# Performance work log

Hardware: AMD Instinct MI355X
Metric: run time of the kernel (lower is better)

Reference implementation:

```python
import jax, jax.numpy as jnp
import numpy as np
from jax import lax

B, C, N, NB = 64, 512, 1024, 4
BC = C // NB
KS = [3, 5, 7, 9]
LEVEL = 2  # min(2, pywt.dwt_max_level(1024, 8)) = 2
FL = 8  # db4 filter length
DN = ('NCH', 'OIH', 'NCH')
# pywt db4 decomposition filters
DEC_LO = jnp.array([-0.010597401784997278, 0.032883011666982945, 0.030841381835986965,
                    -0.18703481171888114, -0.02798376941698385, 0.6308807679295904,
                    0.7148465705525415, 0.23037781330885523], jnp.float32)
DEC_HI = jnp.array([-0.23037781330885523, 0.7148465705525415, -0.6308807679295904,
                    -0.02798376941698385, 0.18703481171888114, 0.030841381835986965,
                    -0.032883011666982945, -0.010597401784997278], jnp.float32)


def conv1d(x, w, b, pad):
    y = lax.conv_general_dilated(x, w, (1,), [(pad, pad)], dimension_numbers=DN)
    return y + b[None, :, None]


def bn_relu(x, g, beta, eps=1e-5):
    # BatchNorm1d in train mode: batch statistics over (B, L) per channel
    mu = x.mean(axis=(0, 2), keepdims=True)
    var = ((x - mu) ** 2).mean(axis=(0, 2), keepdims=True)
    xn = (x - mu) * lax.rsqrt(var + eps)
    return jax.nn.relu(xn * g[None, :, None] + beta[None, :, None])


def dwt1d(x):
    # single-level pywt-compatible DWT, symmetric mode. x: [B, C, n]
    b, c, n = x.shape
    out = (n + FL - 1) // 2
    p = 2 * (out - 1) - n + FL
    xp = jnp.pad(x, ((0, 0), (0, 0), (p // 2, p - p // 2)), mode='symmetric')
    k = jnp.stack([DEC_LO[::-1], DEC_HI[::-1]])[:, None, :]  # [2,1,FL]
    y = lax.conv_general_dilated(xp.reshape(b * c, 1, -1), k, (2,), 'VALID',
                                 dimension_numbers=DN)
    y = y.reshape(b, c, 2, out)
    return y[:, :, 0], y[:, :, 1]  # (cA, cD)


def idwt1d(lo, hi):
    # single-level inverse DWT; output length = 2*nc - FL + 2
    b, c, nc = lo.shape
    x = jnp.stack([lo, hi], axis=2).reshape(b * c, 2, nc)
    # rec filters = dec filters reversed, so flipped-for-conv == dec filters
    k = jnp.stack([DEC_LO, DEC_HI])[None, :, :]  # [1,2,FL]
    y = lax.conv_general_dilated(x, k, (1,), [(FL - 1, FL - 1)],
                                 lhs_dilation=(2,), dimension_numbers=DN)
    y = y[:, 0, FL - 2: FL - 2 + 2 * nc - FL + 2]
    return y.reshape(b, c, -1)


def decouple(x):
    # TemporalPatternDecoupling: db4 wavedec(level=2) -> reconstruct low-pass-only
    # (long term) and detail-only (short term). Torch detaches before pywt.
    x = lax.stop_gradient(x)
    n = x.shape[-1]
    a, details = x, []
    for _ in range(LEVEL):
        a, d = dwt1d(a)
        details.append(d)
    la, sa = a, jnp.zeros_like(a)
    for d in reversed(details):
        dl = d.shape[-1]
        la = idwt1d(la[..., :dl], jnp.zeros_like(d))
        sa = idwt1d(sa[..., :dl], d)
    return sa[..., :n], la[..., :n]


def setup_inputs() -> dict:
    key = jax.random.key(0)
    ks = jax.random.split(key, 32)
    s = 0.05
    inp = {
        'x': jax.random.normal(ks[0], (B, C, N), jnp.float32),
        'w_init': jax.random.normal(ks[1], (C, C, 1), jnp.float32) * s,
        'b_init': jnp.zeros((C,), jnp.float32),
        'w_pf': jax.random.normal(ks[2], (BC, 2 * BC, 1), jnp.float32) * s,
        'b_pf': jnp.zeros((BC,), jnp.float32),
        'w_fus': jax.random.normal(ks[3], (C, C, 1), jnp.float32) * s,
        'b_fus': jnp.zeros((C,), jnp.float32),
    }
    for i in range(NB):
        inp[f'w_b{i + 1}'] = jax.random.normal(ks[4 + i], (BC, BC, KS[i]), jnp.float32) * s
        inp[f'b_b{i + 1}'] = jnp.zeros((BC,), jnp.float32)
        inp[f'g_b{i + 1}'] = jnp.ones((BC,), jnp.float32)
        inp[f'be_b{i + 1}'] = jnp.zeros((BC,), jnp.float32)
    return inp


def reference(x, w_init, b_init, w_b1, b_b1, g_b1, be_b1, w_b2, b_b2, g_b2, be_b2,
              w_b3, b_b3, g_b3, be_b3, w_b4, b_b4, g_b4, be_b4, w_pf, b_pf,
              w_fus, b_fus):
    identity = x
    h = conv1d(x, w_init, b_init, 0)
    branch_in = jnp.split(h, NB, axis=1)
    wb = [w_b1, w_b2, w_b3, w_b4]
    bb = [b_b1, b_b2, b_b3, b_b4]
    gb = [g_b1, g_b2, g_b3, g_b4]
    beb = [be_b1, be_b2, be_b3, be_b4]
    shorts, longs = [], []
    for i in range(NB):
        y = bn_relu(conv1d(branch_in[i], wb[i], bb[i], KS[i] // 2), gb[i], beb[i])
        s, l = decouple(y)
        shorts.append(s)
        longs.append(l)
    for b in range(1, NB):
        shorts[b] = shorts[b] + shorts[b - 1]
    for b in range(NB - 2, -1, -1):
        longs[b] = longs[b] + longs[b + 1]
    enhanced = [conv1d(jnp.concatenate([shorts[b], longs[b]], axis=1), w_pf, b_pf, 0)
                for b in range(NB)]
    out = conv1d(jnp.concatenate(enhanced, axis=1), w_fus, b_fus, 0)
    return out + identity
```

## Files before the change

### kernel.cpp

```cpp
#include <hip/hip_runtime.h>

typedef float  f32x4 __attribute__((ext_vector_type(4)));
typedef short  s16x8 __attribute__((ext_vector_type(8)));
typedef short  s16x4 __attribute__((ext_vector_type(4)));
typedef unsigned short u16;

struct PtrQuad { const float* p[4]; };

__constant__ float c_lo[8] = {-0.010597401784997278f, 0.032883011666982945f,
                              0.030841381835986965f, -0.18703481171888114f,
                              -0.02798376941698385f, 0.6308807679295904f,
                              0.7148465705525415f,  0.23037781330885523f};
__constant__ float c_hi[8] = {-0.23037781330885523f, 0.7148465705525415f,
                              -0.6308807679295904f, -0.02798376941698385f,
                              0.18703481171888114f, 0.030841381835986965f,
                              -0.032883011666982945f, -0.010597401784997278f};

__device__ __forceinline__ u16 f2bf(float f) {
    unsigned u = __float_as_uint(f);
    u += 0x7fffu + ((u >> 16) & 1u);
    return (u16)(u >> 16);
}
__device__ __forceinline__ float bf2f(u16 h) {
    return __uint_as_float(((unsigned)h) << 16);
}
__device__ __forceinline__ int lds_chunk(int row, int g) {
    return row * 4 + (g ^ ((row >> 1) & 3));
}
__device__ __forceinline__ void gload16(void* lds, const void* g) {
    __builtin_amdgcn_global_load_lds(
        (__attribute__((address_space(1))) const void*)g,
        (__attribute__((address_space(3))) void*)lds,
        16, 0, 0);
}
__device__ __forceinline__ void pipe_wait2(int t, int nt) {
    if (t + 1 < nt) asm volatile("s_waitcnt vmcnt(4)" ::: "memory");
    else            asm volatile("s_waitcnt vmcnt(0)" ::: "memory");
    __builtin_amdgcn_s_barrier();
    __builtin_amdgcn_sched_barrier(0);
}
__device__ __forceinline__ void pipe_endbar() {
    __builtin_amdgcn_sched_barrier(0);
    __builtin_amdgcn_s_barrier();
}

__global__ __launch_bounds__(256) void gemm_nt_k(
    const u16* __restrict__ A, long aB, int lda,
    const u16* __restrict__ B, long bB, int ldb,
    int K,
    u16* __restrict__ D, long dB, int dj,
    const float* __restrict__ bias)
{
    __shared__ s16x8 As[2 * 512];
    __shared__ s16x8 Bs[2 * 512];
    int flat = blockIdx.x + 8 * (blockIdx.y + 4 * blockIdx.z);
    int swz = (flat & 7) * 256 + (flat >> 3);
    const int j0 = (swz & 7) * 128;
    const int i0 = ((swz >> 3) & 3) * 128;
    const long bb = swz >> 5;
    const u16* Ab = A + bb * aB;
    const u16* Bb = B + bb * bB;
    const int tid = threadIdx.x;
    const int srow = tid >> 2, sg = tid & 3;
    const int ssg = sg ^ ((srow >> 1) & 3);
    const int l = tid & 63, w = tid >> 6;
    const int wi = (w >> 1) * 64, wj = (w & 1) * 64;
    const int lr = l & 15, lg = l >> 4;
    const long aoff0 = (long)(i0 + srow) * lda + ssg * 8;
    const long aoff1 = (long)(i0 + srow + 64) * lda + ssg * 8;
    const long boff0 = (long)(j0 + srow) * ldb + ssg * 8;
    const long boff1 = (long)(j0 + srow + 64) * ldb + ssg * 8;
    const int nt = K >> 5;
    auto stage = [&](int buf, int t) {
        const int k0 = t << 5;
        char* a0 = (char*)As + buf * 8192 + w * 1024;
        char* b0 = (char*)Bs + buf * 8192 + w * 1024;
        gload16(a0, Ab + aoff0 + k0);
        gload16(a0 + 4096, Ab + aoff1 + k0);
        gload16(b0, Bb + boff0 + k0);
        gload16(b0 + 4096, Bb + boff1 + k0);
    };
    f32x4 acc[4][4] = {};
    stage(0, 0);
    for (int t = 0; t < nt; ++t) {
        const int cur = t & 1;
        if (t + 1 < nt) stage(cur ^ 1, t + 1);
        pipe_wait2(t, nt);
        s16x8 af[4], bf[4];
        #pragma unroll
        for (int f = 0; f < 4; ++f) {
            af[f] = As[cur * 512 + lds_chunk(wi + f * 16 + lr, lg)];
            bf[f] = Bs[cur * 512 + lds_chunk(wj + f * 16 + lr, lg)];
        }
        #pragma unroll
        for (int fi = 0; fi < 4; ++fi)
            #pragma unroll
            for (int fj = 0; fj < 4; ++fj)
                acc[fi][fj] = __builtin_amdgcn_mfma_f32_16x16x32_bf16(af[fi], bf[fj], acc[fi][fj], 0, 0, 0);
        pipe_endbar();
    }
    u16* Db = D + bb * dB;
    #pragma unroll
    for (int fi = 0; fi < 4; ++fi) {
        const int i = i0 + wi + fi * 16 + lg * 4;
        float b0 = 0, b1 = 0, b2v = 0, b3 = 0;
        if (bias) { b0 = bias[i]; b1 = bias[i + 1]; b2v = bias[i + 2]; b3 = bias[i + 3]; }
        #pragma unroll
        for (int fj = 0; fj < 4; ++fj) {
            const int j = j0 + wj + fj * 16 + lr;
            f32x4 d = acc[fi][fj];
            s16x4 o;
            o[0] = (short)f2bf(d[0] + b0); o[1] = (short)f2bf(d[1] + b1);
            o[2] = (short)f2bf(d[2] + b2v); o[3] = (short)f2bf(d[3] + b3);
            *(s16x4*)(Db + (long)j * dj + i) = o;
        }
    }
}

__global__ __launch_bounds__(256) void gemm_branch4_k(
    const u16* __restrict__ WpAll,
    const u16* __restrict__ H,
    u16* __restrict__ Y,
    const u16* __restrict__ zbuf,
    float* __restrict__ part)
{
    __shared__ s16x8 As[2 * 512];
    __shared__ s16x8 Bs[2 * 512];
    __shared__ float sred[2][128];
    __shared__ float qred[2][128];
    int flat = blockIdx.x + 8 * (blockIdx.y + 4 * blockIdx.z);
    int swz = (flat & 7) * 256 + (flat >> 3);
    const int jblk = swz & 7;
    const int br = (swz >> 3) & 3;
    const long bb = swz >> 5;
    const int j0 = jblk * 128;
    const int taps = 3 + 2 * br;
    const int pad = 1 + br;
    const u16* Wp = WpAll + (long)(br * br + 2 * br) * 16384;
    const u16* Hb = H + bb * 524288 + 128 * br;
    const int tid = threadIdx.x;
    const int srow = tid >> 2, sg = tid & 3;
    const int ssg = sg ^ ((srow >> 1) & 3);
    const int l = tid & 63, w = tid >> 6;
    const int wi = (w >> 1) * 64, wj = (w & 1) * 64;
    const int lr = l & 15, lg = l >> 4;
    const int lda = taps * 128;
    const int nt = taps * 4;
    auto stage = [&](int buf, int t) {
        const int k0 = t << 5;
        const int tap = k0 >> 7, kc = k0 & 127;
        const int shift = tap - pad;
        char* a0 = (char*)As + buf * 8192 + w * 1024;
        char* b0 = (char*)Bs + buf * 8192 + w * 1024;
        gload16(a0, Wp + (long)srow * lda + k0 + ssg * 8);
        gload16(a0 + 4096, Wp + (long)(srow + 64) * lda + k0 + ssg * 8);
        int n0r = j0 + srow + shift;
        int n1r = n0r + 64;
        const u16* s0 = (n0r >= 0 && n0r < 1024) ? (Hb + (long)n0r * 512 + kc + ssg * 8) : zbuf;
        const u16* s1 = (n1r >= 0 && n1r < 1024) ? (Hb + (long)n1r * 512 + kc + ssg * 8) : zbuf;
        gload16(b0, s0);
        gload16(b0 + 4096, s1);
    };
    f32x4 acc[4][4] = {};
    stage(0, 0);
    for (int t = 0; t < nt; ++t) {
        const int cur = t & 1;
        if (t + 1 < nt) stage(cur ^ 1, t + 1);
        pipe_wait2(t, nt);
        s16x8 af[4], bf[4];
        #pragma unroll
        for (int f = 0; f < 4; ++f) {
            af[f] = As[cur * 512 + lds_chunk(wi + f * 16 + lr, lg)];
            bf[f] = Bs[cur * 512 + lds_chunk(wj + f * 16 + lr, lg)];
        }
        #pragma unroll
        for (int fi = 0; fi < 4; ++fi)
            #pragma unroll
            for (int fj = 0; fj < 4; ++fj)
                acc[fi][fj] = __builtin_amdgcn_mfma_f32_16x16x32_bf16(af[fi], bf[fj], acc[fi][fj], 0, 0, 0);
        pipe_endbar();
    }
    u16* Db = Y + bb * 524288 + 128 * br;
    #pragma unroll
    for (int fi = 0; fi < 4; ++fi) {
        const int i = wi + fi * 16 + lg * 4;
        #pragma unroll
        for (int fj = 0; fj < 4; ++fj) {
            const int j = j0 + wj + fj * 16 + lr;
            f32x4 d = acc[fi][fj];
            s16x4 o;
            o[0] = (short)f2bf(d[0]); o[1] = (short)f2bf(d[1]);
            o[2] = (short)f2bf(d[2]); o[3] = (short)f2bf(d[3]);
            *(s16x4*)(Db + (long)j * 512 + i) = o;
        }
    }
    float sv[16], qv[16];
    #pragma unroll
    for (int fi = 0; fi < 4; ++fi)
        #pragma unroll
        for (int e = 0; e < 4; ++e) {
            float s = 0.f, q = 0.f;
            #pragma unroll
            for (int fj = 0; fj < 4; ++fj) { float d = acc[fi][fj][e]; s += d; q += d * d; }
            sv[fi * 4 + e] = s; qv[fi * 4 + e] = q;
        }
    #pragma unroll
    for (int m = 1; m < 16; m <<= 1) {
        #pragma unroll
        for (int r = 0; r < 16; ++r) {
            sv[r] += __shfl_xor(sv[r], m, 64);
            qv[r] += __shfl_xor(qv[r], m, 64);
        }
    }
    __syncthreads();
    if (lr == 0) {
        #pragma unroll
        for (int r = 0; r < 16; ++r) {
            int co = wi + (r >> 2) * 16 + lg * 4 + (r & 3);
            sred[w & 1][co] = sv[r];
            qred[w & 1][co] = qv[r];
        }
    }
    __syncthreads();
    if (tid < 128) {
        long blk = (long)br * 512 + bb * 8 + jblk;
        part[blk * 256 + tid]       = sred[0][tid] + sred[1][tid];
        part[blk * 256 + 128 + tid] = qred[0][tid] + qred[1][tid];
    }
}

__global__ __launch_bounds__(256) void gemm_psl_k(
    const u16* __restrict__ Ybn,
    const u16* __restrict__ Bmat,
    u16* __restrict__ PSL)
{
    __shared__ s16x8 As[2 * 512];
    __shared__ s16x8 Bs[2 * 512];
    int flat = blockIdx.x + 8 * (blockIdx.y + 8 * blockIdx.z);
    int swz = (flat & 7) * 512 + (flat >> 3);
    const int j0 = (swz & 7) * 128;
    const int i0 = ((swz >> 3) & 7) * 128;
    const long bb = swz >> 6;
    const int tid = threadIdx.x;
    const u16* Ab = Ybn + bb * 524288;
    const int srow = tid >> 2, sg = tid & 3;
    const int ssg = sg ^ ((srow >> 1) & 3);
    const int l = tid & 63, w = tid >> 6;
    const int wi = (w >> 1) * 64, wj = (w & 1) * 64;
    const int lr = l & 15, lg = l >> 4;
    const long aoff0 = (long)(i0 + srow) * 512 + ssg * 8;
    const long aoff1 = (long)(i0 + srow + 64) * 512 + ssg * 8;
    const long boff0 = (long)(j0 + srow) * 512 + ssg * 8;
    const long boff1 = (long)(j0 + srow + 64) * 512 + ssg * 8;
    const int nt = 16;
    auto stage = [&](int buf, int t) {
        const int k0 = t << 5;
        char* a0 = (char*)As + buf * 8192 + w * 1024;
        char* b0 = (char*)Bs + buf * 8192 + w * 1024;
        gload16(a0, Ab + aoff0 + k0);
        gload16(a0 + 4096, Ab + aoff1 + k0);
        gload16(b0, Bmat + boff0 + k0);
        gload16(b0 + 4096, Bmat + boff1 + k0);
    };
    f32x4 acc[4][4] = {};
    stage(0, 0);
    for (int t = 0; t < nt; ++t) {
        const int cur = t & 1;
        if (t + 1 < nt) stage(cur ^ 1, t + 1);
        pipe_wait2(t, nt);
        s16x8 af[4], bf[4];
        #pragma unroll
        for (int f = 0; f < 4; ++f) {
            af[f] = As[cur * 512 + lds_chunk(wi + f * 16 + lr, lg)];
            bf[f] = Bs[cur * 512 + lds_chunk(wj + f * 16 + lr, lg)];
        }
        #pragma unroll
        for (int fi = 0; fi < 4; ++fi)
            #pragma unroll
            for (int fj = 0; fj < 4; ++fj)
                acc[fi][fj] = __builtin_amdgcn_mfma_f32_16x16x32_bf16(af[fi], bf[fj], acc[fi][fj], 0, 0, 0);
        pipe_endbar();
    }
    u16* Db = PSL + bb * 1048576;
    #pragma unroll
    for (int fi = 0; fi < 4; ++fi) {
        const int i = i0 + wi + fi * 16 + lg * 4;
        #pragma unroll
        for (int fj = 0; fj < 4; ++fj) {
            const int j = j0 + wj + fj * 16 + lr;
            f32x4 d = acc[fi][fj];
            s16x4 o;
            o[0] = (short)f2bf(d[0]); o[1] = (short)f2bf(d[1]);
            o[2] = (short)f2bf(d[2]); o[3] = (short)f2bf(d[3]);
            *(s16x4*)(Db + (long)j * 1024 + i) = o;
        }
    }
}

__global__ __launch_bounds__(256) void gemm_time_k(
    const u16* __restrict__ MS,
    const u16* __restrict__ PSL,
    const float* __restrict__ b2, const float* __restrict__ X,
    float* __restrict__ OUT)
{
    __shared__ s16x8 As[2 * 512];
    __shared__ s16x8 Bs[2 * 512];
    int flat = blockIdx.x + 4 * (blockIdx.y + 8 * blockIdx.z);
    int swz = (flat & 7) * 256 + (flat >> 3);
    const int j0 = (swz & 3) * 128;
    const int i0 = ((swz >> 2) & 7) * 128;
    const long bb = swz >> 5;
    const int tid = threadIdx.x;
    const int srow = tid >> 2, sg = tid & 3;
    const int ssg = sg ^ ((srow >> 1) & 3);
    const int l = tid & 63, w = tid >> 6;
    const int wi = (w >> 1) * 64, wj = (w & 1) * 64;
    const int lr = l & 15, lg = l >> 4;
    const int klo = (i0 - 32) > 0 ? (i0 - 32) : 0;
    const int khi = (i0 + 160) < 1024 ? (i0 + 160) : 1024;
    const int nt = (khi - klo) >> 5;
    const u16* B = PSL + bb * 1048576;
    auto stage = [&](int buf, int t) {
        const int k0 = klo + (t << 5);
        char* a0 = (char*)As + buf * 8192 + w * 1024;
        char* b0 = (char*)Bs + buf * 8192 + w * 1024;
        gload16(a0, MS + (long)(i0 + srow) * 1024 + k0 + ssg * 8);
        gload16(a0 + 4096, MS + (long)(i0 + srow + 64) * 1024 + k0 + ssg * 8);
        gload16(b0, B + (long)(j0 + srow) * 1024 + k0 + ssg * 8);
        gload16(b0 + 4096, B + (long)(j0 + srow + 64) * 1024 + k0 + ssg * 8);
    };
    f32x4 acc[4][4] = {};
    stage(0, 0);
    for (int t = 0; t < nt; ++t) {
        const int cur = t & 1;
        if (t + 1 < nt) stage(cur ^ 1, t + 1);
        pipe_wait2(t, nt);
        s16x8 af[4], bf[4];
        #pragma unroll
        for (int f = 0; f < 4; ++f) {
            af[f] = As[cur * 512 + lds_chunk(wi + f * 16 + lr, lg)];
            bf[f] = Bs[cur * 512 + lds_chunk(wj + f * 16 + lr, lg)];
        }
        #pragma unroll
        for (int fi = 0; fi < 4; ++fi)
            #pragma unroll
            for (int fj = 0; fj < 4; ++fj)
                acc[fi][fj] = __builtin_amdgcn_mfma_f32_16x16x32_bf16(af[fi], bf[fj], acc[fi][fj], 0, 0, 0);
        pipe_endbar();
    }
    float* Ob = OUT + bb * 524288;
    const float* Xb = X + bb * 524288;
    const u16* PLb = PSL + bb * 1048576 + 524288;
    #pragma unroll
    for (int fi = 0; fi < 4; ++fi) {
        const int i = i0 + wi + fi * 16 + lg * 4;
        #pragma unroll
        for (int fj = 0; fj < 4; ++fj) {
            const int j = j0 + wj + fj * 16 + lr;
            const long a = (long)j * 1024 + i;
            f32x4 d = acc[fi][fj];
            const float bj = b2[j];
            f32x4 xv = *(const f32x4*)(Xb + a);
            s16x4 pl4 = *(const s16x4*)(PLb + a);
            f32x4 o;
            o[0] = d[0] + bj + xv[0] + bf2f((u16)pl4[0]);
            o[1] = d[1] + bj + xv[1] + bf2f((u16)pl4[1]);
            o[2] = d[2] + bj + xv[2] + bf2f((u16)pl4[2]);
            o[3] = d[3] + bj + xv[3] + bf2f((u16)pl4[3]);
            *(f32x4*)(Ob + a) = o;
        }
    }
}

__global__ __launch_bounds__(256) void build_M_k(u16* __restrict__ MS)
{
    __shared__ float a1[515], d1[515], a2[261], d2[261], sa1[515];
    const int r = blockIdx.x;
    const int t = threadIdx.x;
    for (int m = t; m < 515; m += 256) {
        float sa = 0.f, sd = 0.f;
        #pragma unroll
        for (int j = 0; j < 8; ++j) {
            int tt = 2 * m + 1 - j;
            tt = (tt < 0) ? (-tt - 1) : tt;
            tt = (tt >= 1024) ? (2047 - tt) : tt;
            if (tt == r) { sa += c_lo[j]; sd += c_hi[j]; }
        }
        a1[m] = sa; d1[m] = sd;
    }
    __syncthreads();
    for (int m = t; m < 261; m += 256) {
        float sa = 0.f, sd = 0.f;
        #pragma unroll
        for (int j = 0; j < 8; ++j) {
            int tt = 2 * m + 1 - j;
            tt = (tt < 0) ? (-tt - 1) : tt;
            tt = (tt >= 515) ? (1029 - tt) : tt;
            float v = a1[tt];
            sa += v * c_lo[j]; sd += v * c_hi[j];
        }
        a2[m] = sa; d2[m] = sd;
    }
    __syncthreads();
    for (int m = t; m < 515; m += 256) {
        float ss = 0.f;
        #pragma unroll
        for (int k = 0; k < 8; ++k) {
            int tt = m + k - 1;
            if (tt & 1) continue;
            int j = tt >> 1;
            if (j < 0 || j >= 261) continue;
            ss += c_hi[k] * d2[j];
        }
        sa1[m] = ss;
    }
    __syncthreads();
    for (int n = t; n < 1024; n += 256) {
        float ss = 0.f;
        #pragma unroll
        for (int k = 0; k < 8; ++k) {
            int tt = n + k - 1;
            if (tt & 1) continue;
            int j = tt >> 1;
            if (j < 0 || j >= 515) continue;
            ss += c_lo[k] * sa1[j] + c_hi[k] * d1[j];
        }
        MS[(long)n * 1024 + r] = f2bf(ss);
    }
}

__global__ __launch_bounds__(256) void pack_weights_k(
    const float* __restrict__ wi,
    const float* __restrict__ b1, const float* __restrict__ b2_,
    const float* __restrict__ b3, const float* __restrict__ b4,
    u16* __restrict__ Wi, u16* __restrict__ Wp)
{
    int i = blockIdx.x * 256 + threadIdx.x;
    if (i < 262144) Wi[i] = f2bf(wi[i]);
    if (i < 393216) {
        int base, taps;
        const float* s;
        if (i < 49152)       { base = 0;      taps = 3; s = b1; }
        else if (i < 131072) { base = 49152;  taps = 5; s = b2_; }
        else if (i < 245760) { base = 131072; taps = 7; s = b3; }
        else                 { base = 245760; taps = 9; s = b4; }
        int rem = i - base;
        int stride = taps * 128;
        int co = rem / stride;
        int r2 = rem - co * stride;
        int tap = r2 >> 7, ci = r2 & 127;
        Wp[i] = f2bf(s[(long)(co * 128 + ci) * taps + tap]);
    }
}

__global__ __launch_bounds__(256) void make_Ucum_k(
    const float* __restrict__ wf, const float* __restrict__ wp,
    u16* __restrict__ UDUL)
{
    int gid = blockIdx.x * 256 + threadIdx.x;
    int co = gid >> 7, cc = gid & 127;
    float us[4], ul[4];
    #pragma unroll
    for (int b = 0; b < 4; ++b) {
        float s = 0.f, t = 0.f;
        for (int q = 0; q < 128; ++q) {
            float f = wf[(long)co * 512 + b * 128 + q];
            s += f * wp[q * 256 + cc];
            t += f * wp[q * 256 + 128 + cc];
        }
        us[b] = s; ul[b] = t;
    }
    float suf[4], pre[4];
    float acc = 0.f;
    for (int b = 3; b >= 0; --b) { acc += us[b]; suf[b] = acc; }
    acc = 0.f;
    for (int b = 0; b < 4; ++b) { acc += ul[b]; pre[b] = acc; }
    #pragma unroll
    for (int b = 0; b < 4; ++b) {
        UDUL[(long)co * 512 + b * 128 + cc]         = f2bf(suf[b] - pre[b]);
        UDUL[(long)(512 + co) * 512 + b * 128 + cc] = f2bf(pre[b]);
    }
}

__global__ __launch_bounds__(256) void make_bias2_k(
    const float* __restrict__ wf, const float* __restrict__ bpf,
    const float* __restrict__ bfus, float* __restrict__ b2)
{
    int co = blockIdx.x * 256 + threadIdx.x;
    if (co >= 512) return;
    float s = bfus[co];
    for (int j = 0; j < 512; ++j) s += wf[(long)co * 512 + j] * bpf[j & 127];
    b2[co] = s;
}

__global__ __launch_bounds__(256) void zero_k(float* __restrict__ p, int n)
{
    int i = blockIdx.x * 256 + threadIdx.x;
    if (i < n) p[i] = 0.f;
}

__global__ __launch_bounds__(256) void trX_k(const float* __restrict__ x, u16* __restrict__ xcl)
{
    __shared__ float sh[32][33];
    const int n0 = blockIdx.x * 32, c0 = blockIdx.y * 32;
    const long bb = blockIdx.z;
    const int tx = threadIdx.x, ty = threadIdx.y;
    const float* xb = x + bb * 524288;
    u16* ob = xcl + bb * 524288;
    #pragma unroll
    for (int k = 0; k < 4; ++k)
        sh[ty + 8 * k][tx] = xb[(long)(c0 + ty + 8 * k) * 1024 + n0 + tx];
    __syncthreads();
    #pragma unroll
    for (int k = 0; k < 4; ++k)
        ob[(long)(n0 + ty + 8 * k) * 512 + c0 + tx] = f2bf(sh[tx][ty + 8 * k]);
}

__global__ __launch_bounds__(256) void bn_coef_k(
    const float* __restrict__ part, PtrQuad g, PtrQuad be, float* __restrict__ scsh)
{
    int c = blockIdx.x * 256 + threadIdx.x;
    if (c >= 512) return;
    int br = c >> 7, cc = c & 127;
    const float* pb = part + (long)br * 131072;
    float s = 0.f, q = 0.f;
    for (int pidx = 0; pidx < 512; ++pidx) {
        s += pb[pidx * 256 + cc];
        q += pb[pidx * 256 + 128 + cc];
    }
    float mu = s * (1.0f / 65536.0f);
    float var = q * (1.0f / 65536.0f) - mu * mu;
    float sc = g.p[br][cc] * rsqrtf(var + 1e-5f);
    scsh[c] = sc;
    scsh[512 + c] = be.p[br][cc] - mu * sc;
}

__global__ __launch_bounds__(256) void bn_apply_k(
    u16* __restrict__ Y, const float* __restrict__ scsh)
{
    __shared__ float sc_[512];
    __shared__ float sh_[512];
    const int t = threadIdx.x;
    #pragma unroll
    for (int q = 0; q < 2; ++q) {
        sc_[t + q * 256] = scsh[t + q * 256];
        sh_[t + q * 256] = scsh[512 + t + q * 256];
    }
    __syncthreads();
    long gid = (long)blockIdx.x * 256 + t;
    long r = gid >> 6; int cg = (int)(gid & 63);
    u16* p = Y + r * 512 + cg * 8;
    s16x8 v = *(const s16x8*)p;
    #pragma unroll
    for (int e = 0; e < 8; ++e) {
        int c = cg * 8 + e;
        float f = bf2f((u16)v[e]) * sc_[c] + sh_[c];
        v[e] = (short)f2bf(f > 0.f ? f : 0.f);
    }
    *(s16x8*)p = v;
}

extern "C" void kernel_launch(void* const* d_in, const int* in_sizes, int n_in,
                              void* d_out, int out_size, void* d_ws, size_t ws_size,
                              hipStream_t stream)
{
    const float* x      = (const float*)d_in[0];
    const float* w_init = (const float*)d_in[1];
    const float* b_init = (const float*)d_in[2];
    const float* w_pf   = (const float*)d_in[3];
    const float* b_pf   = (const float*)d_in[4];
    const float* w_fus  = (const float*)d_in[5];
    const float* b_fus  = (const float*)d_in[6];
    const float *w_b[4];
    PtrQuad g, be;
    for (int i = 0; i < 4; ++i) {
        w_b[i]  = (const float*)d_in[7 + 4 * i];
        g.p[i]  = (const float*)d_in[9 + 4 * i];
        be.p[i] = (const float*)d_in[10 + 4 * i];
    }
    float* outf = (float*)d_out;

    char* p = (char*)d_ws;
    u16* xcl   = (u16*)p;  p += 67108864;
    u16* h     = (u16*)p;  p += 67108864;
    u16* Y     = (u16*)p;  p += 67108864;
    u16* PSL   = (u16*)p;  p += 134217728;
    u16* Wi    = (u16*)p;  p += 524288;
    u16* Wp    = (u16*)p;  p += 786432;
    u16* UDUL  = (u16*)p;  p += 1048576;
    u16* MrowS = (u16*)p;  p += 2097152;
    float* b2  = (float*)p; p += 2048;
    float* zbuf= (float*)p; p += 256;
    float* scsh= (float*)p; p += 4096;
    float* part= (float*)p; p += 2097152;

    pack_weights_k<<<1536, 256, 0, stream>>>(w_init, w_b[0], w_b[1], w_b[2], w_b[3], Wi, Wp);
    make_Ucum_k<<<256, 256, 0, stream>>>(w_fus, w_pf, UDUL);
    make_bias2_k<<<2, 256, 0, stream>>>(w_fus, b_pf, b_fus, b2);
    build_M_k<<<1024, 256, 0, stream>>>(MrowS);
    zero_k<<<1, 256, 0, stream>>>(zbuf, 64);

    trX_k<<<dim3(32, 16, 64), dim3(32, 8), 0, stream>>>(x, xcl);

    gemm_nt_k<<<dim3(8, 4, 64), 256, 0, stream>>>(Wi, 0, 512, xcl, 524288, 512, 512,
                                                  h, 524288, 512, b_init);

    gemm_branch4_k<<<dim3(8, 4, 64), 256, 0, stream>>>(Wp, h, Y, (const u16*)zbuf, part);

    bn_coef_k<<<2, 256, 0, stream>>>(part, g, be, scsh);
    bn_apply_k<<<16384, 256, 0, stream>>>(Y, scsh);

    gemm_psl_k<<<dim3(8, 8, 64), 256, 0, stream>>>(Y, UDUL, PSL);

    gemm_time_k<<<dim3(4, 8, 64), 256, 0, stream>>>(MrowS, PSL, b2, x, outf);
}
```

Measured before the change: 503.7 us.

## Reuse H window across conv taps, parallelize BN stats, raise MFMA priority

Measured after the change: 476.5 us. -5.4%, faster.

```diff
diff --git a/kernel.cpp b/kernel.cpp
--- a/kernel.cpp
+++ b/kernel.cpp
@@ -92,11 +92,13 @@
             af[f] = As[cur * 512 + lds_chunk(wi + f * 16 + lr, lg)];
             bf[f] = Bs[cur * 512 + lds_chunk(wj + f * 16 + lr, lg)];
         }
+        __builtin_amdgcn_s_setprio(1);
         #pragma unroll
         for (int fi = 0; fi < 4; ++fi)
             #pragma unroll
             for (int fj = 0; fj < 4; ++fj)
                 acc[fi][fj] = __builtin_amdgcn_mfma_f32_16x16x32_bf16(af[fi], bf[fj], acc[fi][fj], 0, 0, 0);
+        __builtin_amdgcn_s_setprio(0);
         pipe_endbar();
     }
     u16* Db = D + bb * dB;
@@ -124,8 +126,8 @@
     const u16* __restrict__ zbuf,
     float* __restrict__ part)
 {
-    __shared__ s16x8 As[2 * 512];
-    __shared__ s16x8 Bs[2 * 512];
+    __shared__ char Alds[2 * 8192];
+    __shared__ char Blds[2 * 12288];
     __shared__ float sred[2][128];
     __shared__ float qred[2][128];
     int flat = blockIdx.x + 8 * (blockIdx.y + 4 * blockIdx.z);
@@ -136,49 +138,78 @@
     const int j0 = jblk * 128;
     const int taps = 3 + 2 * br;
     const int pad = 1 + br;
-    const u16* Wp = WpAll + (long)(br * br + 2 * br) * 16384;
+    const u16* Wpb = WpAll + (long)(br * br + 2 * br) * 16384;
     const u16* Hb = H + bb * 524288 + 128 * br;
     const int tid = threadIdx.x;
-    const int srow = tid >> 2, sg = tid & 3;
-    const int ssg = sg ^ ((srow >> 1) & 3);
     const int l = tid & 63, w = tid >> 6;
     const int wi = (w >> 1) * 64, wj = (w & 1) * 64;
     const int lr = l & 15, lg = l >> 4;
+    const int lrow = l >> 2, lq = l & 3;
+    const int ssg2 = lq ^ ((lrow >> 1) & 3);
     const int lda = taps * 128;
-    const int nt = taps * 4;
-    auto stage = [&](int buf, int t) {
-        const int k0 = t << 5;
-        const int tap = k0 >> 7, kc = k0 & 127;
-        const int shift = tap - pad;
-        char* a0 = (char*)As + buf * 8192 + w * 1024;
-        char* b0 = (char*)Bs + buf * 8192 + w * 1024;
-        gload16(a0, Wp + (long)srow * lda + k0 + ssg * 8);
-        gload16(a0 + 4096, Wp + (long)(srow + 64) * lda + k0 + ssg * 8);
-        int n0r = j0 + srow + shift;
-        int n1r = n0r + 64;
-        const u16* s0 = (n0r >= 0 && n0r < 1024) ? (Hb + (long)n0r * 512 + kc + ssg * 8) : zbuf;
-        const u16* s1 = (n1r >= 0 && n1r < 1024) ? (Hb + (long)n1r * 512 + kc + ssg * 8) : zbuf;
-        gload16(b0, s0);
-        gload16(b0 + 4096, s1);
+
+    auto stageA = [&](int buf, int c, int t) {
+        char* dst = Alds + buf * 8192 + w * 2048;
+        #pragma unroll
+        for (int q = 0; q < 2; ++q) {
+            int row = w * 32 + q * 16 + lrow;
+            gload16(dst + q * 1024,
+                    Wpb + (long)row * lda + t * 128 + c * 32 + ssg2 * 8);
+        }
     };
+    auto stageB = [&](int buf, int c) {
+        char* dst = Blds + buf * 12288 + w * 3072;
+        #pragma unroll
+        for (int q = 0; q < 3; ++q) {
+            int winrow = w * 48 + q * 16 + lrow;
+            int grow = j0 - 32 + winrow;
+            const u16* src = (grow >= 0 && grow < 1024)
+                           ? (Hb + (long)grow * 512 + c * 32 + ssg2 * 8) : zbuf;
+            gload16(dst + q * 1024, src);
+        }
+    };
+
     f32x4 acc[4][4] = {};
-    stage(0, 0);
-    for (int t = 0; t < nt; ++t) {
-        const int cur = t & 1;
-        if (t + 1 < nt) stage(cur ^ 1, t + 1);
-        pipe_wait2(t, nt);
-        s16x8 af[4], bf[4];
-        #pragma unroll
-        for (int f = 0; f < 4; ++f) {
-            af[f] = As[cur * 512 + lds_chunk(wi + f * 16 + lr, lg)];
-            bf[f] = Bs[cur * 512 + lds_chunk(wj + f * 16 + lr, lg)];
-        }
-        #pragma unroll
-        for (int fi = 0; fi < 4; ++fi)
+    int abuf = 0, bbuf = 0;
+    stageB(0, 0);
+    stageA(0, 0, 0);
+    for (int c = 0; c < 4; ++c) {
+        for (int t = 0; t < taps; ++t) {
+            if (t + 1 < taps) {
+                stageA(abuf ^ 1, c, t + 1);
+                asm volatile("s_waitcnt vmcnt(2)" ::: "memory");
+            } else if (c + 1 < 4) {
+                stageB(bbuf ^ 1, c + 1);
+                stageA(abuf ^ 1, c + 1, 0);
+                asm volatile("s_waitcnt vmcnt(5)" ::: "memory");
+            } else {
+                asm volatile("s_waitcnt vmcnt(0)" ::: "memory");
+            }
+            __builtin_amdgcn_s_barrier();
+            __builtin_amdgcn_sched_barrier(0);
+            const char* Al = Alds + abuf * 8192;
+            const char* Bl = Blds + bbuf * 12288;
+            const int shift2 = t - pad + 32;
+            s16x8 af[4], bf[4];
             #pragma unroll
-            for (int fj = 0; fj < 4; ++fj)
-                acc[fi][fj] = __builtin_amdgcn_mfma_f32_16x16x32_bf16(af[fi], bf[fj], acc[fi][fj], 0, 0, 0);
-        pipe_endbar();
+            for (int f = 0; f < 4; ++f) {
+                int arow = wi + f * 16 + lr;
+                af[f] = *(const s16x8*)(Al + arow * 64 + (lg ^ ((arow >> 1) & 3)) * 16);
+                int brow = wj + f * 16 + lr + shift2;
+                bf[f] = *(const s16x8*)(Bl + brow * 64 + (lg ^ ((brow >> 1) & 3)) * 16);
+            }
+            __builtin_amdgcn_s_setprio(1);
+            #pragma unroll
+            for (int fi = 0; fi < 4; ++fi)
+                #pragma unroll
+                for (int fj = 0; fj < 4; ++fj)
+                    acc[fi][fj] = __builtin_amdgcn_mfma_f32_16x16x32_bf16(af[fi], bf[fj], acc[fi][fj], 0, 0, 0);
+            __builtin_amdgcn_s_setprio(0);
+            __builtin_amdgcn_sched_barrier(0);
+            __builtin_amdgcn_s_barrier();
+            abuf ^= 1;
+            if (t == taps - 1) bbuf ^= 1;
+        }
     }
     u16* Db = Y + bb * 524288 + 128 * br;
     #pragma unroll
@@ -274,11 +305,13 @@
             af[f] = As[cur * 512 + lds_chunk(wi + f * 16 + lr, lg)];
             bf[f] = Bs[cur * 512 + lds_chunk(wj + f * 16 + lr, lg)];
         }
+        __builtin_amdgcn_s_setprio(1);
         #pragma unroll
         for (int fi = 0; fi < 4; ++fi)
             #pragma unroll
             for (int fj = 0; fj < 4; ++fj)
                 acc[fi][fj] = __builtin_amdgcn_mfma_f32_16x16x32_bf16(af[fi], bf[fj], acc[fi][fj], 0, 0, 0);
+        __builtin_amdgcn_s_setprio(0);
         pipe_endbar();
     }
     u16* Db = PSL + bb * 1048576;
@@ -341,11 +374,13 @@
             af[f] = As[cur * 512 + lds_chunk(wi + f * 16 + lr, lg)];
             bf[f] = Bs[cur * 512 + lds_chunk(wj + f * 16 + lr, lg)];
         }
+        __builtin_amdgcn_s_setprio(1);
         #pragma unroll
         for (int fi = 0; fi < 4; ++fi)
             #pragma unroll
             for (int fj = 0; fj < 4; ++fj)
                 acc[fi][fj] = __builtin_amdgcn_mfma_f32_16x16x32_bf16(af[fi], bf[fj], acc[fi][fj], 0, 0, 0);
+        __builtin_amdgcn_s_setprio(0);
         pipe_endbar();
     }
     float* Ob = OUT + bb * 524288;
@@ -519,20 +554,26 @@
 __global__ __launch_bounds__(256) void bn_coef_k(
     const float* __restrict__ part, PtrQuad g, PtrQuad be, float* __restrict__ scsh)
 {
-    int c = blockIdx.x * 256 + threadIdx.x;
-    if (c >= 512) return;
+    __shared__ float rs[256], rq[256];
+    int c = blockIdx.x;
     int br = c >> 7, cc = c & 127;
     const float* pb = part + (long)br * 131072;
-    float s = 0.f, q = 0.f;
-    for (int pidx = 0; pidx < 512; ++pidx) {
-        s += pb[pidx * 256 + cc];
-        q += pb[pidx * 256 + 128 + cc];
-    }
-    float mu = s * (1.0f / 65536.0f);
-    float var = q * (1.0f / 65536.0f) - mu * mu;
-    float sc = g.p[br][cc] * rsqrtf(var + 1e-5f);
-    scsh[c] = sc;
-    scsh[512 + c] = be.p[br][cc] - mu * sc;
+    int t = threadIdx.x;
+    float s = pb[(2 * t) * 256 + cc]       + pb[(2 * t + 1) * 256 + cc];
+    float q = pb[(2 * t) * 256 + 128 + cc] + pb[(2 * t + 1) * 256 + 128 + cc];
+    rs[t] = s; rq[t] = q;
+    __syncthreads();
+    for (int off = 128; off > 0; off >>= 1) {
+        if (t < off) { rs[t] += rs[t + off]; rq[t] += rq[t + off]; }
+        __syncthreads();
+    }
+    if (t == 0) {
+        float mu = rs[0] * (1.0f / 65536.0f);
+        float var = rq[0] * (1.0f / 65536.0f) - mu * mu;
+        float sc = g.p[br][cc] * rsqrtf(var + 1e-5f);
+        scsh[c] = sc;
+        scsh[512 + c] = be.p[br][cc] - mu * sc;
+    }
 }
 
 __global__ __launch_bounds__(256) void bn_apply_k(
@@ -607,7 +648,7 @@
 
     gemm_branch4_k<<<dim3(8, 4, 64), 256, 0, stream>>>(Wp, h, Y, (const u16*)zbuf, part);
 
-    bn_coef_k<<<2, 256, 0, stream>>>(part, g, be, scsh);
+    bn_coef_k<<<512, 256, 0, stream>>>(part, g, be, scsh);
     bn_apply_k<<<16384, 256, 0, stream>>>(Y, scsh);
 
     gemm_psl_k<<<dim3(8, 8, 64), 256, 0, stream>>>(Y, UDUL, PSL);
```
